# Kernel optimization log

Measured on AMD Instinct MI355X. Metric: run time of the kernel, lower is better.

The kernel has to match this reference:

```python
import jax, jax.numpy as jnp
import numpy as np
import math

N_CHANNELS = 256
D_K = 64
N_HEADS = N_CHANNELS // D_K  # 4
N_GROUPS = 32
EPS = 1e-5
SCALE = 1.0 / math.sqrt(math.sqrt(D_K))


def setup_inputs() -> dict:
    key = jax.random.key(0)
    ks = jax.random.split(key, 7)
    B, C, H, W = 2, N_CHANNELS, 64, 64
    inner = N_HEADS * D_K
    x = jax.random.normal(ks[0], (B, C, H, W), dtype=jnp.float32)
    gn_w = jnp.ones((C,), dtype=jnp.float32)
    gn_b = jnp.zeros((C,), dtype=jnp.float32)
    proj_w = jax.random.normal(ks[1], (3 * inner, C), dtype=jnp.float32) / math.sqrt(C)
    proj_b = jnp.zeros((3 * inner,), dtype=jnp.float32)
    out_w = jax.random.normal(ks[2], (C, inner), dtype=jnp.float32) / math.sqrt(inner)
    out_b = jnp.zeros((C,), dtype=jnp.float32)
    return {"x": x, "gn_w": gn_w, "gn_b": gn_b, "proj_w": proj_w,
            "proj_b": proj_b, "out_w": out_w, "out_b": out_b}


def _group_norm(x, gamma, beta):
    # x: [B, C, H, W], 32 groups, affine per channel
    B, C, H, W = x.shape
    xg = x.reshape(B, N_GROUPS, C // N_GROUPS, H * W)
    mean = xg.mean(axis=(2, 3), keepdims=True)
    var = xg.var(axis=(2, 3), keepdims=True)
    xn = (xg - mean) * jax.lax.rsqrt(var + EPS)
    xn = xn.reshape(B, C, H, W)
    return xn * gamma[None, :, None, None] + beta[None, :, None, None]


def reference(x, gn_w, gn_b, proj_w, proj_b, out_w, out_b):
    B, C, H, W = x.shape
    S = H * W
    h = _group_norm(x, gn_w, gn_b).reshape(B, C, S).transpose(0, 2, 1)  # [B, S, C]
    qkv = h @ proj_w.T + proj_b                                          # [B, S, 3*nh*dk]
    qkv = qkv.reshape(B, S, N_HEADS, 3 * D_K)
    q, k, v = jnp.split(qkv, 3, axis=-1)                                 # [B, S, nh, dk] each
    # bihd,bjhd->bijh with scale applied to both q and k (net 1/sqrt(dk))
    attn = jnp.einsum('bihd,bjhd->bijh', q * SCALE, k * SCALE)
    attn = jax.nn.softmax(attn, axis=2)
    res = jnp.einsum('bijh,bjhd->bihd', attn, v).reshape(B, S, N_HEADS * D_K)
    res = res @ out_w.T + out_b                                          # [B, S, C]
    res = res.transpose(0, 2, 1).reshape(B, C, H, W)
    return res + x
```

## Files before the change

### kernel.cpp

```cpp
#include <hip/hip_runtime.h>
#include <math.h>

#define NB 2
#define NC 256
#define NS 4096
#define NG 32
#define CPG 8
#define NH 4
#define DK 64
#define NQKV 768
#define NKG 4
#define TPG 8
#define QS 0.18033688011112042f

typedef __attribute__((ext_vector_type(8))) short short8;
typedef __attribute__((ext_vector_type(4))) float f32x4;
typedef __attribute__((ext_vector_type(16))) float f32x16;
typedef __attribute__((ext_vector_type(2))) unsigned uint2v;
typedef __attribute__((ext_vector_type(4))) unsigned uint4v;

union U8 { uint4v u; short8 s; };

__device__ __forceinline__ short f2bf(float f){
  union { float f; unsigned u; } v; v.f = f;
  unsigned r = v.u + 0x7fffu + ((v.u >> 16) & 1u);
  return (short)(r >> 16);
}
__device__ __forceinline__ float bf2f(short s){
  union { unsigned u; float f; } v; v.u = ((unsigned)(unsigned short)s) << 16; return v.f;
}
__device__ __forceinline__ float ex2(float x){
  float y; asm("v_exp_f32 %0, %1" : "=v"(y) : "v"(x)); return y;
}
__device__ __forceinline__ unsigned cvtpk(float lo, float hi){
  unsigned u; asm("v_cvt_pk_bf16_f32 %0, %1, %2" : "=v"(u) : "v"(lo), "v"(hi)); return u;
}
__device__ __forceinline__ void pl32swap(unsigned &x, unsigned &y){
  asm("v_permlane32_swap_b32 %0, %1" : "+v"(x), "+v"(y));
}

__global__ __launch_bounds__(256) void k_prep(const float* __restrict__ x,
                                              const float* __restrict__ pw,
                                              const float* __restrict__ ow,
                                              const float* __restrict__ gw,
                                              const float* __restrict__ gb,
                                              short* __restrict__ h,
                                              short* __restrict__ pwb,
                                              short* __restrict__ owb){
  int bk = blockIdx.x;
  int tid = threadIdx.x;
  if (bk < 64){
    int b = bk >> 5, g = bk & 31;
    const float* base = x + (size_t)bk*(CPG*NS);
    const f32x4* b4 = (const f32x4*)base;
    float s = 0.f, ss = 0.f;
    for (int i = tid; i < (CPG*NS)/4; i += 256){
      f32x4 v = b4[i];
      s  += (v[0]+v[1])+(v[2]+v[3]);
      ss += (v[0]*v[0]+v[1]*v[1])+(v[2]*v[2]+v[3]*v[3]);
    }
    for (int o = 32; o > 0; o >>= 1){ s += __shfl_down(s,o); ss += __shfl_down(ss,o); }
    __shared__ float red[8];
    __shared__ float mrs[2];
    int w = tid >> 6;
    if ((tid & 63) == 0){ red[w] = s; red[4+w] = ss; }
    __syncthreads();
    if (tid == 0){
      float S  = red[0]+red[1]+red[2]+red[3];
      float SS = red[4]+red[5]+red[6]+red[7];
      const float inv = 1.f/(float)(CPG*NS);
      float m = S*inv; float var = SS*inv - m*m;
      mrs[0] = m; mrs[1] = rsqrtf(var + 1e-5f);
    }
    __syncthreads();
    float mu = mrs[0], rs = mrs[1];
    float wv[8], bv[8];
    #pragma unroll
    for (int c = 0; c < 8; ++c){
      wv[c] = gw[g*8 + c] * rs;
      bv[c] = gb[g*8 + c] - mu * wv[c];
    }
    short* hb = h + (size_t)b*NS*NC + g*8;
    for (int i = tid; i < NS; i += 256){
      unsigned u[4];
      #pragma unroll
      for (int c2 = 0; c2 < 4; ++c2){
        float v0 = base[(size_t)(2*c2  )*NS + i]*wv[2*c2  ] + bv[2*c2  ];
        float v1 = base[(size_t)(2*c2+1)*NS + i]*wv[2*c2+1] + bv[2*c2+1];
        u[c2] = cvtpk(v0, v1);
      }
      *(uint4v*)&hb[(size_t)i*NC] = (uint4v){u[0],u[1],u[2],u[3]};
    }
  } else {
    int i = (bk - 64)*256 + tid;
    if (i < NQKV*NC) pwb[i] = f2bf(pw[i]);
    if (i < NC*NC)   owb[i] = f2bf(ow[i]);
  }
}

__global__ __launch_bounds__(256) void k_qkv(const short* __restrict__ h,
                                             const short* __restrict__ wb,
                                             const float* __restrict__ pb,
                                             short* __restrict__ qo,
                                             short* __restrict__ ko,
                                             short* __restrict__ vto){
  __shared__ short As[64][72];
  __shared__ short Bs[128][72];
  int m0 = blockIdx.x << 6;
  int n0 = blockIdx.y << 7;
  int tid = threadIdx.x;
  int lane = tid & 63, wid = tid >> 6;
  int wm = (wid >> 1) << 5, wn = (wid & 1) << 6;
  int l15 = lane & 15, lg = lane >> 4;
  const f32x4 fz = {0.f,0.f,0.f,0.f};
  f32x4 acc[2][4];
  for (int i=0;i<2;i++) for(int j=0;j<4;j++) acc[i][j] = fz;
  for (int k0 = 0; k0 < NC; k0 += 64){
    __syncthreads();
    for (int it = 0; it < 2; ++it){
      int c = it*256 + tid;
      int r = c >> 3, ch = (c & 7) << 3;
      *(short8*)&As[r][ch] = *(const short8*)&h[((size_t)(m0 + r))*NC + k0 + ch];
    }
    for (int it = 0; it < 4; ++it){
      int c = it*256 + tid;
      int r = c >> 3, ch = (c & 7) << 3;
      *(short8*)&Bs[r][ch] = *(const short8*)&wb[((size_t)(n0 + r))*NC + k0 + ch];
    }
    __syncthreads();
    #pragma unroll
    for (int kk = 0; kk < 2; ++kk){
      short8 a[2], b[4];
      for (int mf=0; mf<2; ++mf) a[mf] = *(const short8*)&As[wm + mf*16 + l15][kk*32 + lg*8];
      for (int nf=0; nf<4; ++nf) b[nf] = *(const short8*)&Bs[wn + nf*16 + l15][kk*32 + lg*8];
      for (int mf=0; mf<2; ++mf)
        for (int nf=0; nf<4; ++nf)
          acc[mf][nf] = __builtin_amdgcn_mfma_f32_16x16x32_bf16(a[mf], b[nf], acc[mf][nf], 0,0,0);
    }
  }
  for (int mf=0; mf<2; ++mf)
    for (int nf=0; nf<4; ++nf)
      for (int r=0; r<4; ++r){
        int m = m0 + wm + mf*16 + lg*4 + r;
        int o = n0 + wn + nf*16 + l15;
        float val = acc[mf][nf][r] + pb[o];
        int b_ = m >> 12, s = m & 4095;
        int hh = o / 192, rem = o - hh*192;
        int t = rem >> 6, d = rem & 63;
        size_t bh = (size_t)(b_*NH + hh);
        if (t == 0)      qo [(bh*NS + s)*DK + d] = f2bf(val * QS);
        else if (t == 1) ko [(bh*NS + s)*DK + d] = f2bf(val);
        else             vto[(bh*DK + d)*NS + s] = f2bf(val);
      }
}

struct SMK1 { short kv[NKG][2][64][72]; };
struct SMCH {
  float gOB[3][4][32][33];
  float mlh[3][4][2][32];
  float fOB[4][32][33];
};

__global__ __launch_bounds__(1024, 4) void k_attn(const short* __restrict__ q,
                                                  const short* __restrict__ k,
                                                  const short* __restrict__ vt,
                                                  short* __restrict__ op,
                                                  float* __restrict__ mlp){
  extern __shared__ char smem[];
  SMK1* sk = (SMK1*)smem;
  SMCH* sc = (SMCH*)smem;

  int blk = blockIdx.x;
  int bh   = blk & 7;
  int rest = blk >> 3;
  int qi   = rest & 31;
  int kvh  = rest >> 5;
  int q0   = qi << 7;
  const short* Qb = q  + (size_t)bh*NS*DK;
  const short* Kb = k  + (size_t)bh*NS*DK;
  const short* Vb = vt + (size_t)bh*DK*NS;
  int tid = threadIdx.x, lane = tid & 63, wid = tid >> 6;
  int l31 = lane & 31, hi = lane >> 5;
  int g = wid >> 2, wq = wid & 3;
  int gtid = tid & 255;
  int kvbase = kvh*2048 + g*512;

  short8 bq[4];
  {
    const short* qrow = Qb + (size_t)(q0 + wq*32 + l31)*DK + hi*8;
    #pragma unroll
    for (int s2 = 0; s2 < 4; ++s2) bq[s2] = *(const short8*)(qrow + s2*16);
  }

  f32x16 ot0, ot1;
  #pragma unroll
  for (int i = 0; i < 16; ++i){ ot0[i] = 0.f; ot1[i] = 0.f; }
  float mrun = -1e30f, lrun = 0.f;

  short8 kpre[2], vpre[2];
  #pragma unroll
  for (int it = 0; it < 2; ++it){
    int c = it*256 + gtid, r = c >> 3, col = (c & 7) << 3;
    kpre[it] = *(const short8*)&Kb[(size_t)(kvbase + r)*DK + col];
    vpre[it] = *(const short8*)&Vb[(size_t)r*NS + kvbase + col];
  }
  #pragma unroll
  for (int it = 0; it < 2; ++it){
    int c = it*256 + gtid, r = c >> 3, col = (c & 7) << 3;
    *(short8*)&sk->kv[g][0][r][col] = kpre[it];
    *(short8*)&sk->kv[g][1][r][col] = vpre[it];
  }
  #pragma unroll
  for (int it = 0; it < 2; ++it){
    int c = it*256 + gtid, r = c >> 3, col = (c & 7) << 3;
    kpre[it] = *(const short8*)&Kb[(size_t)(kvbase + 64 + r)*DK + col];
    vpre[it] = *(const short8*)&Vb[(size_t)r*NS + kvbase + 64 + col];
  }

  for (int t = 0; t < TPG; ++t){
    __syncthreads();
    const short (*Kl)[72] = sk->kv[g][0];
    const short (*Vl)[72] = sk->kv[g][1];
    f32x16 st0, st1;
    #pragma unroll
    for (int i = 0; i < 16; ++i){ st0[i] = 0.f; st1[i] = 0.f; }
    const short* Kr0 = &Kl[l31][hi*8];
    const short* Kr1 = &Kl[32 + l31][hi*8];
    #pragma unroll
    for (int s2 = 0; s2 < 4; ++s2){
      short8 ka0 = *(const short8*)(Kr0 + s2*16);
      short8 ka1 = *(const short8*)(Kr1 + s2*16);
      st0 = __builtin_amdgcn_mfma_f32_32x32x16_bf16(ka0, bq[s2], st0, 0,0,0);
      st1 = __builtin_amdgcn_mfma_f32_32x32x16_bf16(ka1, bq[s2], st1, 0,0,0);
    }
    float mx = -1e30f;
    #pragma unroll
    for (int i = 0; i < 16; ++i) mx = fmaxf(mx, fmaxf(st0[i], st1[i]));
    mx = fmaxf(mx, __shfl_xor(mx, 32));
    if (!__all(mx - mrun <= 8.f)){
      float mnew = fmaxf(mrun, mx);
      float corr = ex2(mrun - mnew);
      lrun *= corr;
      #pragma unroll
      for (int i = 0; i < 16; ++i){ ot0[i] *= corr; ot1[i] *= corr; }
      mrun = mnew;
    }
    float p0[16], p1[16]; float ps = 0.f;
    #pragma unroll
    for (int i = 0; i < 16; ++i){
      p0[i] = ex2(st0[i] - mrun); p1[i] = ex2(st1[i] - mrun);
      ps += p0[i] + p1[i];
    }
    ps += __shfl_xor(ps, 32);
    lrun += ps;
    unsigned pk0[8], pk1[8];
    #pragma unroll
    for (int a = 0; a < 4; ++a){
      pk0[a]     = cvtpk(p0[4*a+0], p0[4*a+1]);
      pk1[a]     = cvtpk(p0[4*a+2], p0[4*a+3]);
      pk0[4 + a] = cvtpk(p1[4*a+0], p1[4*a+1]);
      pk1[4 + a] = cvtpk(p1[4*a+2], p1[4*a+3]);
    }
    const short* Vr0 = &Vl[l31][hi*8];
    const short* Vr1 = &Vl[32 + l31][hi*8];
    #pragma unroll
    for (int i2 = 0; i2 < 4; ++i2){
      unsigned w0 = pk0[2*i2], w2 = pk0[2*i2+1]; pl32swap(w0, w2);
      unsigned w1 = pk1[2*i2], w3 = pk1[2*i2+1]; pl32swap(w1, w3);
      U8 cv; cv.u = (uint4v){w0, w1, w2, w3};
      short8 av0 = *(const short8*)(Vr0 + i2*16);
      short8 av1 = *(const short8*)(Vr1 + i2*16);
      ot0 = __builtin_amdgcn_mfma_f32_32x32x16_bf16(av0, cv.s, ot0, 0,0,0);
      ot1 = __builtin_amdgcn_mfma_f32_32x32x16_bf16(av1, cv.s, ot1, 0,0,0);
    }
    __syncthreads();
    if (t + 1 < TPG){
      #pragma unroll
      for (int it = 0; it < 2; ++it){
        int c = it*256 + gtid, r = c >> 3, col = (c & 7) << 3;
        *(short8*)&sk->kv[g][0][r][col] = kpre[it];
        *(short8*)&sk->kv[g][1][r][col] = vpre[it];
      }
    }
    if (t + 2 < TPG){
      int kv0 = kvbase + (t + 2)*64;
      #pragma unroll
      for (int it = 0; it < 2; ++it){
        int c = it*256 + gtid, r = c >> 3, col = (c & 7) << 3;
        kpre[it] = *(const short8*)&Kb[(size_t)(kv0 + r)*DK + col];
        vpre[it] = *(const short8*)&Vb[(size_t)r*NS + kv0 + col];
      }
    }
  }

  size_t pbase = ((size_t)(bh*2 + kvh)*NS + q0);
  float w0 = 1.f, w1 = 0.f, w2 = 0.f, w3 = 0.f;
  __syncthreads();
  if (g > 0){
    #pragma unroll
    for (int r2 = 0; r2 < 16; ++r2){
      int dl = (r2 & 3) + 8*(r2 >> 2) + 4*hi;
      sc->gOB[g-1][wq][dl][l31] = ot0[r2];
    }
    if (hi == 0){ sc->mlh[g-1][wq][0][l31] = mrun; sc->mlh[g-1][wq][1][l31] = lrun; }
  }
  __syncthreads();
  if (g == 0){
    float m1 = sc->mlh[0][wq][0][l31], l1 = sc->mlh[0][wq][1][l31];
    float m2 = sc->mlh[1][wq][0][l31], l2 = sc->mlh[1][wq][1][l31];
    float m3 = sc->mlh[2][wq][0][l31], l3 = sc->mlh[2][wq][1][l31];
    float M  = fmaxf(fmaxf(mrun, m1), fmaxf(m2, m3));
    w0 = ex2(mrun - M); w1 = ex2(m1 - M); w2 = ex2(m2 - M); w3 = ex2(m3 - M);
    float L = lrun*w0 + l1*w1 + l2*w2 + l3*w3;
    #pragma unroll
    for (int r2 = 0; r2 < 16; ++r2){
      int dl = (r2 & 3) + 8*(r2 >> 2) + 4*hi;
      sc->fOB[wq][dl][l31] = ot0[r2]*w0 + sc->gOB[0][wq][dl][l31]*w1
                           + sc->gOB[1][wq][dl][l31]*w2 + sc->gOB[2][wq][dl][l31]*w3;
    }
    if (hi == 0){
      size_t mi = (pbase + wq*32 + l31)*2;
      mlp[mi] = M; mlp[mi+1] = L;
    }
  }
  __syncthreads();
  {
    int row = tid >> 3, dc = (tid & 7) << 2;
    float v0 = sc->fOB[row >> 5][dc+0][row & 31];
    float v1 = sc->fOB[row >> 5][dc+1][row & 31];
    float v2 = sc->fOB[row >> 5][dc+2][row & 31];
    float v3 = sc->fOB[row >> 5][dc+3][row & 31];
    uint2v pv = { cvtpk(v0,v1), cvtpk(v2,v3) };
    *(uint2v*)&op[(pbase + row)*DK + dc] = pv;
  }
  __syncthreads();
  if (g > 0){
    #pragma unroll
    for (int r2 = 0; r2 < 16; ++r2){
      int dl = (r2 & 3) + 8*(r2 >> 2) + 4*hi;
      sc->gOB[g-1][wq][dl][l31] = ot1[r2];
    }
  }
  __syncthreads();
  if (g == 0){
    #pragma unroll
    for (int r2 = 0; r2 < 16; ++r2){
      int dl = (r2 & 3) + 8*(r2 >> 2) + 4*hi;
      sc->fOB[wq][dl][l31] = ot1[r2]*w0 + sc->gOB[0][wq][dl][l31]*w1
                           + sc->gOB[1][wq][dl][l31]*w2 + sc->gOB[2][wq][dl][l31]*w3;
    }
  }
  __syncthreads();
  {
    int row = tid >> 3, dc = (tid & 7) << 2;
    float v0 = sc->fOB[row >> 5][dc+0][row & 31];
    float v1 = sc->fOB[row >> 5][dc+1][row & 31];
    float v2 = sc->fOB[row >> 5][dc+2][row & 31];
    float v3 = sc->fOB[row >> 5][dc+3][row & 31];
    uint2v pv = { cvtpk(v0,v1), cvtpk(v2,v3) };
    *(uint2v*)&op[(pbase + row)*DK + 32 + dc] = pv;
  }
}

__global__ __launch_bounds__(256) void k_out(const short* __restrict__ op,
                                             const float* __restrict__ mlp,
                                             const short* __restrict__ wb,
                                             const float* __restrict__ ob,
                                             const float* __restrict__ x,
                                             float* __restrict__ out){
  __shared__ short As[64][40];
  __shared__ short Bs[64][40];
  __shared__ float wgt[4][64][2];
  int m0 = blockIdx.x << 6;
  int n0 = blockIdx.y << 6;
  int b = m0 >> 12, srow0 = m0 & 4095;
  int tid = threadIdx.x;
  {
    int s_rel = tid >> 2, hh = tid & 3;
    size_t base0 = ((size_t)((b*4 + hh)*2 + 0)*NS + srow0 + s_rel)*2;
    size_t base1 = ((size_t)((b*4 + hh)*2 + 1)*NS + srow0 + s_rel)*2;
    float m0v = mlp[base0], l0v = mlp[base0+1];
    float m1v = mlp[base1], l1v = mlp[base1+1];
    float M = fmaxf(m0v, m1v);
    float a0 = ex2(m0v - M), a1 = ex2(m1v - M);
    float inv = 1.f/(l0v*a0 + l1v*a1);
    wgt[hh][s_rel][0] = a0*inv;
    wgt[hh][s_rel][1] = a1*inv;
  }
  int lane = tid & 63, wid = tid >> 6;
  int wm = (wid >> 1) << 5, wn = (wid & 1) << 5;
  int l15 = lane & 15, lg = lane >> 4;
  const f32x4 fz = {0.f,0.f,0.f,0.f};
  f32x4 acc[2][2];
  for (int i=0;i<2;i++) for(int j=0;j<2;j++) acc[i][j] = fz;
  for (int k0 = 0; k0 < NC; k0 += 32){
    __syncthreads();
    {
      int c = tid;
      int r = c >> 2, kk8 = (c & 3) << 3;
      int hh = k0 >> 6, dbase = (k0 & 63) + kk8;
      size_t o0i = ((size_t)((b*4 + hh)*2 + 0)*NS + srow0 + r)*DK + dbase;
      size_t o1i = ((size_t)((b*4 + hh)*2 + 1)*NS + srow0 + r)*DK + dbase;
      short8 o0 = *(const short8*)&op[o0i];
      short8 o1 = *(const short8*)&op[o1i];
      float w0v = wgt[hh][r][0], w1v = wgt[hh][r][1];
      unsigned pk[4];
      #pragma unroll
      for (int j2 = 0; j2 < 4; ++j2){
        float f0 = bf2f(o0[2*j2  ])*w0v + bf2f(o1[2*j2  ])*w1v;
        float f1 = bf2f(o0[2*j2+1])*w0v + bf2f(o1[2*j2+1])*w1v;
        pk[j2] = cvtpk(f0, f1);
      }
      *(uint4v*)&As[r][kk8] = (uint4v){pk[0],pk[1],pk[2],pk[3]};
      *(short8*)&Bs[r][kk8] = *(const short8*)&wb[((size_t)(n0 + r))*NC + k0 + kk8];
    }
    __syncthreads();
    short8 a[2], bfr[2];
    for (int mf=0; mf<2; ++mf) a[mf]   = *(const short8*)&As[wm + mf*16 + l15][lg*8];
    for (int nf=0; nf<2; ++nf) bfr[nf] = *(const short8*)&Bs[wn + nf*16 + l15][lg*8];
    for (int mf=0; mf<2; ++mf)
      for (int nf=0; nf<2; ++nf)
        acc[mf][nf] = __builtin_amdgcn_mfma_f32_16x16x32_bf16(a[mf], bfr[nf], acc[mf][nf], 0,0,0);
  }
  for (int mf=0; mf<2; ++mf)
    for (int nf=0; nf<2; ++nf)
      for (int r=0; r<4; ++r){
        int m = m0 + wm + mf*16 + lg*4 + r;
        int o = n0 + wn + nf*16 + l15;
        int b_ = m >> 12, s = m & 4095;
        size_t idx = ((size_t)b_*NC + o)*NS + s;
        out[idx] = acc[mf][nf][r] + ob[o] + x[idx];
      }
}

extern "C" void kernel_launch(void* const* d_in, const int* in_sizes, int n_in,
                              void* d_out, int out_size, void* d_ws, size_t ws_size,
                              hipStream_t stream){
  const float* x   = (const float*)d_in[0];
  const float* gnw = (const float*)d_in[1];
  const float* gnb = (const float*)d_in[2];
  const float* pw  = (const float*)d_in[3];
  const float* pb  = (const float*)d_in[4];
  const float* ow  = (const float*)d_in[5];
  const float* ob  = (const float*)d_in[6];
  float* out = (float*)d_out;

  char* ws = (char*)d_ws;
  short* wqkv = (short*)(ws + 512);
  short* wout = wqkv + NQKV*NC;
  short* h    = wout + NC*NC;
  short* qb   = h   + (size_t)NB*NS*NC;
  short* kb   = qb  + (size_t)NB*NH*NS*DK;
  short* vtb  = kb  + (size_t)NB*NH*NS*DK;
  short* opb  = vtb + (size_t)NB*NH*NS*DK;
  float* mlb  = (float*)(opb + (size_t)8*2*NS*DK);

  k_prep<<<832, 256, 0, stream>>>(x, pw, ow, gnw, gnb, h, wqkv, wout);
  k_qkv<<<dim3(128, 6), 256, 0, stream>>>(h, wqkv, pb, qb, kb, vtb);
  k_attn<<<512, 1024, sizeof(SMK1), stream>>>(qb, kb, vtb, opb, mlb);
  k_out<<<dim3(128, 4), 256, 0, stream>>>(opb, mlb, wout, ob, x, out);
}
```

Measured before the change: 105.7 us.

## Split attention KV range four ways across smaller blocks and merge in output kernel

The attention kernel moves from 1024-thread blocks with four in-block KV groups and two KV halves to 512-thread blocks with two in-block KV groups and four KV quarters across blocks. The grid doubles and each block's in-block reduction and shared memory shrink. The output projection kernel now merges four partial results per row using their max and sum statistics, reading twice as much partial-output data. The partial-output buffer reuses the normalized-activation workspace, and the partial writes use wider 16-byte stores.

```diff
diff --git a/kernel.cpp b/kernel.cpp
--- a/kernel.cpp
+++ b/kernel.cpp
@@ -9,7 +9,7 @@
 #define NH 4
 #define DK 64
 #define NQKV 768
-#define NKG 4
+#define NKH 4
 #define TPG 8
 #define QS 0.18033688011112042f
 
@@ -154,18 +154,18 @@
       }
 }
 
-struct SMK1 { short kv[NKG][2][64][72]; };
+struct SMK1 { short kv[2][2][64][72]; };
 struct SMCH {
-  float gOB[3][4][32][33];
-  float mlh[3][4][2][32];
+  float gOB[4][32][33];
+  float mlh[4][2][32];
   float fOB[4][32][33];
 };
 
-__global__ __launch_bounds__(1024, 4) void k_attn(const short* __restrict__ q,
-                                                  const short* __restrict__ k,
-                                                  const short* __restrict__ vt,
-                                                  short* __restrict__ op,
-                                                  float* __restrict__ mlp){
+__global__ __launch_bounds__(512, 4) void k_attn(const short* __restrict__ q,
+                                                 const short* __restrict__ k,
+                                                 const short* __restrict__ vt,
+                                                 short* __restrict__ op,
+                                                 float* __restrict__ mlp){
   extern __shared__ char smem[];
   SMK1* sk = (SMK1*)smem;
   SMCH* sc = (SMCH*)smem;
@@ -183,7 +183,7 @@
   int l31 = lane & 31, hi = lane >> 5;
   int g = wid >> 2, wq = wid & 3;
   int gtid = tid & 255;
-  int kvbase = kvh*2048 + g*512;
+  int kvbase = kvh*1024 + g*512;
 
   short8 bq[4];
   {
@@ -293,30 +293,27 @@
     }
   }
 
-  size_t pbase = ((size_t)(bh*2 + kvh)*NS + q0);
-  float w0 = 1.f, w1 = 0.f, w2 = 0.f, w3 = 0.f;
-  __syncthreads();
-  if (g > 0){
+  size_t pbase = ((size_t)(bh*4 + kvh)*NS + q0);
+  float w0 = 1.f, w1 = 0.f;
+  __syncthreads();
+  if (g == 1){
     #pragma unroll
     for (int r2 = 0; r2 < 16; ++r2){
       int dl = (r2 & 3) + 8*(r2 >> 2) + 4*hi;
-      sc->gOB[g-1][wq][dl][l31] = ot0[r2];
-    }
-    if (hi == 0){ sc->mlh[g-1][wq][0][l31] = mrun; sc->mlh[g-1][wq][1][l31] = lrun; }
+      sc->gOB[wq][dl][l31] = ot0[r2];
+    }
+    if (hi == 0){ sc->mlh[wq][0][l31] = mrun; sc->mlh[wq][1][l31] = lrun; }
   }
   __syncthreads();
   if (g == 0){
-    float m1 = sc->mlh[0][wq][0][l31], l1 = sc->mlh[0][wq][1][l31];
-    float m2 = sc->mlh[1][wq][0][l31], l2 = sc->mlh[1][wq][1][l31];
-    float m3 = sc->mlh[2][wq][0][l31], l3 = sc->mlh[2][wq][1][l31];
-    float M  = fmaxf(fmaxf(mrun, m1), fmaxf(m2, m3));
-    w0 = ex2(mrun - M); w1 = ex2(m1 - M); w2 = ex2(m2 - M); w3 = ex2(m3 - M);
-    float L = lrun*w0 + l1*w1 + l2*w2 + l3*w3;
+    float m1 = sc->mlh[wq][0][l31], l1 = sc->mlh[wq][1][l31];
+    float M  = fmaxf(mrun, m1);
+    w0 = ex2(mrun - M); w1 = ex2(m1 - M);
+    float L = lrun*w0 + l1*w1;
     #pragma unroll
     for (int r2 = 0; r2 < 16; ++r2){
       int dl = (r2 & 3) + 8*(r2 >> 2) + 4*hi;
-      sc->fOB[wq][dl][l31] = ot0[r2]*w0 + sc->gOB[0][wq][dl][l31]*w1
-                           + sc->gOB[1][wq][dl][l31]*w2 + sc->gOB[2][wq][dl][l31]*w3;
+      sc->fOB[wq][dl][l31] = ot0[r2]*w0 + sc->gOB[wq][dl][l31]*w1;
     }
     if (hi == 0){
       size_t mi = (pbase + wq*32 + l31)*2;
@@ -325,20 +322,20 @@
   }
   __syncthreads();
   {
-    int row = tid >> 3, dc = (tid & 7) << 2;
-    float v0 = sc->fOB[row >> 5][dc+0][row & 31];
-    float v1 = sc->fOB[row >> 5][dc+1][row & 31];
-    float v2 = sc->fOB[row >> 5][dc+2][row & 31];
-    float v3 = sc->fOB[row >> 5][dc+3][row & 31];
-    uint2v pv = { cvtpk(v0,v1), cvtpk(v2,v3) };
-    *(uint2v*)&op[(pbase + row)*DK + dc] = pv;
-  }
-  __syncthreads();
-  if (g > 0){
+    int row = tid >> 2, dc = (tid & 3) << 3;
+    float v2[8];
+    #pragma unroll
+    for (int i = 0; i < 8; ++i) v2[i] = sc->fOB[row >> 5][dc + i][row & 31];
+    uint4v pv = { cvtpk(v2[0],v2[1]), cvtpk(v2[2],v2[3]),
+                  cvtpk(v2[4],v2[5]), cvtpk(v2[6],v2[7]) };
+    *(uint4v*)&op[(pbase + row)*DK + dc] = pv;
+  }
+  __syncthreads();
+  if (g == 1){
     #pragma unroll
     for (int r2 = 0; r2 < 16; ++r2){
       int dl = (r2 & 3) + 8*(r2 >> 2) + 4*hi;
-      sc->gOB[g-1][wq][dl][l31] = ot1[r2];
+      sc->gOB[wq][dl][l31] = ot1[r2];
     }
   }
   __syncthreads();
@@ -346,19 +343,18 @@
     #pragma unroll
     for (int r2 = 0; r2 < 16; ++r2){
       int dl = (r2 & 3) + 8*(r2 >> 2) + 4*hi;
-      sc->fOB[wq][dl][l31] = ot1[r2]*w0 + sc->gOB[0][wq][dl][l31]*w1
-                           + sc->gOB[1][wq][dl][l31]*w2 + sc->gOB[2][wq][dl][l31]*w3;
+      sc->fOB[wq][dl][l31] = ot1[r2]*w0 + sc->gOB[wq][dl][l31]*w1;
     }
   }
   __syncthreads();
   {
-    int row = tid >> 3, dc = (tid & 7) << 2;
-    float v0 = sc->fOB[row >> 5][dc+0][row & 31];
-    float v1 = sc->fOB[row >> 5][dc+1][row & 31];
-    float v2 = sc->fOB[row >> 5][dc+2][row & 31];
-    float v3 = sc->fOB[row >> 5][dc+3][row & 31];
-    uint2v pv = { cvtpk(v0,v1), cvtpk(v2,v3) };
-    *(uint2v*)&op[(pbase + row)*DK + 32 + dc] = pv;
+    int row = tid >> 2, dc = (tid & 3) << 3;
+    float v2[8];
+    #pragma unroll
+    for (int i = 0; i < 8; ++i) v2[i] = sc->fOB[row >> 5][dc + i][row & 31];
+    uint4v pv = { cvtpk(v2[0],v2[1]), cvtpk(v2[2],v2[3]),
+                  cvtpk(v2[4],v2[5]), cvtpk(v2[6],v2[7]) };
+    *(uint4v*)&op[(pbase + row)*DK + 32 + dc] = pv;
   }
 }
 
@@ -370,22 +366,24 @@
                                              float* __restrict__ out){
   __shared__ short As[64][40];
   __shared__ short Bs[64][40];
-  __shared__ float wgt[4][64][2];
+  __shared__ float wgt[4][64][4];
   int m0 = blockIdx.x << 6;
   int n0 = blockIdx.y << 6;
   int b = m0 >> 12, srow0 = m0 & 4095;
   int tid = threadIdx.x;
   {
     int s_rel = tid >> 2, hh = tid & 3;
-    size_t base0 = ((size_t)((b*4 + hh)*2 + 0)*NS + srow0 + s_rel)*2;
-    size_t base1 = ((size_t)((b*4 + hh)*2 + 1)*NS + srow0 + s_rel)*2;
-    float m0v = mlp[base0], l0v = mlp[base0+1];
-    float m1v = mlp[base1], l1v = mlp[base1+1];
-    float M = fmaxf(m0v, m1v);
-    float a0 = ex2(m0v - M), a1 = ex2(m1v - M);
-    float inv = 1.f/(l0v*a0 + l1v*a1);
-    wgt[hh][s_rel][0] = a0*inv;
-    wgt[hh][s_rel][1] = a1*inv;
+    float mv[4], lv[4];
+    #pragma unroll
+    for (int j = 0; j < 4; ++j){
+      size_t bj = ((size_t)((b*4 + hh)*4 + j)*NS + srow0 + s_rel)*2;
+      mv[j] = mlp[bj]; lv[j] = mlp[bj+1];
+    }
+    float M = fmaxf(fmaxf(mv[0], mv[1]), fmaxf(mv[2], mv[3]));
+    float a0 = ex2(mv[0]-M), a1 = ex2(mv[1]-M), a2 = ex2(mv[2]-M), a3 = ex2(mv[3]-M);
+    float inv = 1.f/(lv[0]*a0 + lv[1]*a1 + lv[2]*a2 + lv[3]*a3);
+    wgt[hh][s_rel][0] = a0*inv; wgt[hh][s_rel][1] = a1*inv;
+    wgt[hh][s_rel][2] = a2*inv; wgt[hh][s_rel][3] = a3*inv;
   }
   int lane = tid & 63, wid = tid >> 6;
   int wm = (wid >> 1) << 5, wn = (wid & 1) << 5;
@@ -399,18 +397,20 @@
       int c = tid;
       int r = c >> 2, kk8 = (c & 3) << 3;
       int hh = k0 >> 6, dbase = (k0 & 63) + kk8;
-      size_t o0i = ((size_t)((b*4 + hh)*2 + 0)*NS + srow0 + r)*DK + dbase;
-      size_t o1i = ((size_t)((b*4 + hh)*2 + 1)*NS + srow0 + r)*DK + dbase;
-      short8 o0 = *(const short8*)&op[o0i];
-      short8 o1 = *(const short8*)&op[o1i];
-      float w0v = wgt[hh][r][0], w1v = wgt[hh][r][1];
+      float f[8];
+      #pragma unroll
+      for (int e = 0; e < 8; ++e) f[e] = 0.f;
+      #pragma unroll
+      for (int j = 0; j < 4; ++j){
+        size_t oi = ((size_t)((b*4 + hh)*4 + j)*NS + srow0 + r)*DK + dbase;
+        short8 o = *(const short8*)&op[oi];
+        float wv = wgt[hh][r][j];
+        #pragma unroll
+        for (int e = 0; e < 8; ++e) f[e] += bf2f(o[e])*wv;
+      }
       unsigned pk[4];
       #pragma unroll
-      for (int j2 = 0; j2 < 4; ++j2){
-        float f0 = bf2f(o0[2*j2  ])*w0v + bf2f(o1[2*j2  ])*w1v;
-        float f1 = bf2f(o0[2*j2+1])*w0v + bf2f(o1[2*j2+1])*w1v;
-        pk[j2] = cvtpk(f0, f1);
-      }
+      for (int j2 = 0; j2 < 4; ++j2) pk[j2] = cvtpk(f[2*j2], f[2*j2+1]);
       *(uint4v*)&As[r][kk8] = (uint4v){pk[0],pk[1],pk[2],pk[3]};
       *(short8*)&Bs[r][kk8] = *(const short8*)&wb[((size_t)(n0 + r))*NC + k0 + kk8];
     }
@@ -448,15 +448,15 @@
   char* ws = (char*)d_ws;
   short* wqkv = (short*)(ws + 512);
   short* wout = wqkv + NQKV*NC;
-  short* h    = wout + NC*NC;
-  short* qb   = h   + (size_t)NB*NS*NC;
+  short* qb   = wout + NC*NC;
   short* kb   = qb  + (size_t)NB*NH*NS*DK;
   short* vtb  = kb  + (size_t)NB*NH*NS*DK;
-  short* opb  = vtb + (size_t)NB*NH*NS*DK;
-  float* mlb  = (float*)(opb + (size_t)8*2*NS*DK);
+  short* h    = vtb + (size_t)NB*NH*NS*DK;
+  short* opb  = h;
+  float* mlb  = (float*)(opb + (size_t)8*NKH*NS*DK);
 
   k_prep<<<832, 256, 0, stream>>>(x, pw, ow, gnw, gnb, h, wqkv, wout);
   k_qkv<<<dim3(128, 6), 256, 0, stream>>>(h, wqkv, pb, qb, kb, vtb);
-  k_attn<<<512, 1024, sizeof(SMK1), stream>>>(qb, kb, vtb, opb, mlb);
+  k_attn<<<1024, 512, sizeof(SMK1), stream>>>(qb, kb, vtb, opb, mlb);
   k_out<<<dim3(128, 4), 256, 0, stream>>>(opb, mlb, wout, ob, x, out);
 }
```

Result: no change. 105.4 us (-0.3%).
